# Kernel tuning notes

Hardware: AMD Instinct MI355X
Metric: run time of the kernel (lower is better)

The kernel has to match this reference:

```python
import jax, jax.numpy as jnp
import numpy as np

D_MODEL = 1024
N_HEADS = 16
HEAD_DIM = D_MODEL // N_HEADS


def setup_inputs() -> dict:
    key = jax.random.key(0)
    ks = jax.random.split(key, 9)
    B, S = 4, 2048
    x = jax.random.normal(ks[0], (B, S, D_MODEL), dtype=jnp.float32)
    init = 1.0 / np.sqrt(D_MODEL)
    def lin(kw, kb):
        W = jax.random.uniform(kw, (D_MODEL, D_MODEL), jnp.float32, -init, init)
        b = jax.random.uniform(kb, (D_MODEL,), jnp.float32, -init, init)
        return W, b
    Wq, bq = lin(ks[1], ks[2])
    Wk, bk = lin(ks[3], ks[4])
    Wv, bv = lin(ks[5], ks[6])
    Wo, bo = lin(ks[7], ks[8])
    return {"x": x, "Wq": Wq, "bq": bq, "Wk": Wk, "bk": bk,
            "Wv": Wv, "bv": bv, "Wo": Wo, "bo": bo}


def reference(x, Wq, bq, Wk, bk, Wv, bv, Wo, bo):
    B, S, _ = x.shape
    scale = jnp.sqrt(jnp.float32(HEAD_DIM))
    def split_heads(t):  # [B,S,D] -> [B,H,S,hd]
        return t.reshape(B, S, N_HEADS, HEAD_DIM).transpose(0, 2, 1, 3)
    q = split_heads(x @ Wq.T + bq)
    k = split_heads(x @ Wk.T + bk)
    v = split_heads(x @ Wv.T + bv)
    attn = jnp.einsum('bhqd,bhkd->bhqk', q, k) / scale
    attn = jax.nn.softmax(attn, axis=-1)
    out = jnp.einsum('bhqk,bhkd->bhqd', attn, v)  # [B,H,S,hd]
    out = out.transpose(0, 2, 1, 3).reshape(B, S, D_MODEL)
    return out @ Wo.T + bo
```

## Files before the change

### kernel.cpp

```cpp
#include <hip/hip_runtime.h>
#include <hip/hip_bf16.h>
#include <stdint.h>

typedef __attribute__((ext_vector_type(8))) short bf16x8;
typedef __attribute__((ext_vector_type(4))) float f32x4;
typedef __attribute__((ext_vector_type(16))) float f32x16;
typedef __attribute__((ext_vector_type(2))) unsigned int u32x2;
typedef unsigned short u16;

#define DEVI static __device__ __forceinline__

DEVI u16 f2bf(float f) {
  union { float f; uint32_t u; } x; x.f = f;
  uint32_t r = (x.u + 0x7FFFu + ((x.u >> 16) & 1u)) >> 16;
  return (u16)r;
}

DEVI void gload_lds16(const void* g, void* lds) {
  __builtin_amdgcn_global_load_lds(
      (const __attribute__((address_space(1))) void*)(void*)g,
      (__attribute__((address_space(3))) void*)lds, 16, 0, 0);
}

DEVI unsigned ldsaddr(const void* p) { return (unsigned)(uintptr_t)p; }

__global__ void cvt_all_kernel(const float* __restrict__ x,
                               const float* __restrict__ Wq, const float* __restrict__ Wk,
                               const float* __restrict__ Wv, const float* __restrict__ Wo,
                               const float* __restrict__ bq, const float* __restrict__ bk,
                               const float* __restrict__ bv,
                               u16* __restrict__ xb, u16* __restrict__ Wqkvb,
                               u16* __restrict__ Wob, float* __restrict__ bqkv) {
  const int X4 = 2097152;
  const int W4 = 262144;
  const int total = X4 + 4 * W4 + 768;
  int i = blockIdx.x * blockDim.x + threadIdx.x;
  const int stride = gridDim.x * blockDim.x;
  for (; i < total; i += stride) {
    if (i < X4) {
      float4 v = ((const float4*)x)[i];
      ((ushort4*)xb)[i] = make_ushort4(f2bf(v.x), f2bf(v.y), f2bf(v.z), f2bf(v.w));
    } else if (i < X4 + 4 * W4) {
      int j = i - X4;
      int which = j >> 18;
      int o = j & (W4 - 1);
      const float* src = which == 0 ? Wq : which == 1 ? Wk : which == 2 ? Wv : Wo;
      u16* dst = (which == 3) ? Wob : (Wqkvb + (size_t)which * 1048576);
      float4 v = ((const float4*)src)[o];
      ((ushort4*)dst)[o] = make_ushort4(f2bf(v.x), f2bf(v.y), f2bf(v.z), f2bf(v.w));
    } else {
      int j = i - X4 - 4 * W4;
      int which = j >> 8;
      int o = j & 255;
      const float* src = which == 0 ? bq : which == 1 ? bk : bv;
      ((float4*)bqkv)[which * 256 + o] = ((const float4*)src)[o];
    }
  }
}

template<int OUT_BF16>
__global__ __launch_bounds__(256, 2)
void gemm_bt_kernel(const u16* __restrict__ A, const u16* __restrict__ B,
                    const float* __restrict__ bias, void* __restrict__ C,
                    int M, int N, int K, int scale_cols, float scale_val) {
  __shared__ u16 As[128 * 32];
  __shared__ u16 Bs[128 * 32];
  const int tid = threadIdx.x;
  const int l = tid & 63;
  const int w = tid >> 6;
  const int bm = blockIdx.y, bn = blockIdx.x;
  const int wm = w >> 1, wn = w & 1;

  f32x4 acc[4][4] = {};

  const int srow = w * 32 + (l >> 2);
  const int scol = (l & 3) * 8;
  const u16* gA0 = A + (size_t)(bm * 128 + srow) * K + scol;
  const u16* gA1 = gA0 + (size_t)16 * K;
  const u16* gB0 = B + (size_t)(bn * 128 + srow) * K + scol;
  const u16* gB1 = gB0 + (size_t)16 * K;
  u16* lA0 = As + w * 1024;
  u16* lA1 = As + w * 1024 + 512;
  u16* lB0 = Bs + w * 1024;
  u16* lB1 = Bs + w * 1024 + 512;

  const int ar = wm * 64 + (l & 15);
  const int br = wn * 64 + (l & 15);
  const int kb = (l >> 4) * 8;

  for (int k0 = 0; k0 < K; k0 += 32) {
    __syncthreads();
    gload_lds16(gA0 + k0, lA0);
    gload_lds16(gA1 + k0, lA1);
    gload_lds16(gB0 + k0, lB0);
    gload_lds16(gB1 + k0, lB1);
    __syncthreads();
    bf16x8 af[4], bfr[4];
#pragma unroll
    for (int mf = 0; mf < 4; ++mf)
      af[mf] = *(const bf16x8*)&As[(ar + mf * 16) * 32 + kb];
#pragma unroll
    for (int nf = 0; nf < 4; ++nf)
      bfr[nf] = *(const bf16x8*)&Bs[(br + nf * 16) * 32 + kb];
#pragma unroll
    for (int mf = 0; mf < 4; ++mf)
#pragma unroll
      for (int nf = 0; nf < 4; ++nf)
        acc[mf][nf] = __builtin_amdgcn_mfma_f32_16x16x32_bf16(af[mf], bfr[nf], acc[mf][nf], 0, 0, 0);
  }

  const int rbase = bm * 128 + wm * 64 + (l >> 4) * 4;
  const int cbase = bn * 128 + wn * 64 + (l & 15);
#pragma unroll
  for (int nf = 0; nf < 4; ++nf) {
    int col = cbase + nf * 16;
    float bsv = bias[col];
    float sc = (col < scale_cols) ? scale_val : 1.0f;
#pragma unroll
    for (int mf = 0; mf < 4; ++mf) {
#pragma unroll
      for (int j = 0; j < 4; ++j) {
        int row = rbase + mf * 16 + j;
        float v = (acc[mf][nf][j] + bsv) * sc;
        if (OUT_BF16) ((u16*)C)[(size_t)row * N + col] = f2bf(v);
        else          ((float*)C)[(size_t)row * N + col] = v;
      }
    }
  }
}

DEVI void softmax_pa(f32x16& sA, f32x16& sB, bf16x8* pa, float& lsum, int hi) {
  float rs = 0.f;
#pragma unroll
  for (int r = 0; r < 16; ++r) { sA[r] = __builtin_amdgcn_exp2f(sA[r]); rs += sA[r]; }
#pragma unroll
  for (int r = 0; r < 16; ++r) { sB[r] = __builtin_amdgcn_exp2f(sB[r]); rs += sB[r]; }
  lsum += rs + __shfl_xor(rs, 32, 64);
#pragma unroll
  for (int i = 0; i < 4; ++i) {
    float p0 = (8 * i + 0 < 16) ? sA[(8 * i + 0) & 15] : sB[(8 * i + 0) & 15];
    float p1 = (8 * i + 1 < 16) ? sA[(8 * i + 1) & 15] : sB[(8 * i + 1) & 15];
    float p2 = (8 * i + 2 < 16) ? sA[(8 * i + 2) & 15] : sB[(8 * i + 2) & 15];
    float p3 = (8 * i + 3 < 16) ? sA[(8 * i + 3) & 15] : sB[(8 * i + 3) & 15];
    float p4 = (8 * i + 4 < 16) ? sA[(8 * i + 4) & 15] : sB[(8 * i + 4) & 15];
    float p5 = (8 * i + 5 < 16) ? sA[(8 * i + 5) & 15] : sB[(8 * i + 5) & 15];
    float p6 = (8 * i + 6 < 16) ? sA[(8 * i + 6) & 15] : sB[(8 * i + 6) & 15];
    float p7 = (8 * i + 7 < 16) ? sA[(8 * i + 7) & 15] : sB[(8 * i + 7) & 15];
    unsigned a0, a1, b0, b1;
    asm("v_cvt_pk_bf16_f32 %0, %1, %2" : "=v"(a0) : "v"(p0), "v"(p1));
    asm("v_cvt_pk_bf16_f32 %0, %1, %2" : "=v"(a1) : "v"(p2), "v"(p3));
    asm("v_cvt_pk_bf16_f32 %0, %1, %2" : "=v"(b0) : "v"(p4), "v"(p5));
    asm("v_cvt_pk_bf16_f32 %0, %1, %2" : "=v"(b1) : "v"(p6), "v"(p7));
    unsigned t0 = hi ? a0 : b0;
    unsigned t1 = hi ? a1 : b1;
    unsigned x0 = (unsigned)__shfl_xor((int)t0, 32, 64);
    unsigned x1 = (unsigned)__shfl_xor((int)t1, 32, 64);
    union { unsigned u[4]; bf16x8 v; } U;
    U.u[0] = hi ? x0 : a0;
    U.u[1] = hi ? x1 : a1;
    U.u[2] = hi ? b0 : x0;
    U.u[3] = hi ? b1 : x1;
    pa[i] = U.v;
  }
}

__global__ __launch_bounds__(256, 2)
void attn_kernel(const u16* __restrict__ QKV, u16* __restrict__ O) {
  __shared__ u16 Ks[2][4096];
  __shared__ u16 Vs[2][4096];

  const int tid = threadIdx.x;
  const int l = tid & 63, w = tid >> 6;
  const int hi = l >> 5, c = l & 31;
  const int bh = blockIdx.y, b = bh >> 4, h = bh & 15;
  const int qb = blockIdx.x * 256 + w * 64;
  const size_t rowbase = (size_t)b * 2048;

  bf16x8 qf0[4], qf1[4];
  {
    const u16* Qp0 = QKV + (rowbase + qb + c) * 3072 + h * 64 + hi * 8;
    const u16* Qp1 = QKV + (rowbase + qb + 32 + c) * 3072 + h * 64 + hi * 8;
#pragma unroll
    for (int kk = 0; kk < 4; ++kk) {
      qf0[kk] = *(const bf16x8*)(Qp0 + kk * 16);
      qf1[kk] = *(const bf16x8*)(Qp1 + kk * 16);
    }
  }

  const int kd0 = (w * 2 + 0) * 64 + l;
  const int kd1 = (w * 2 + 1) * 64 + l;
  const int rK0 = kd0 >> 3, dbK0 = (kd0 & 7) ^ (rK0 & 7);
  const int rK1 = kd1 >> 3, dbK1 = (kd1 & 7) ^ (rK1 & 7);
  const u16* srcK0 = QKV + (rowbase + rK0) * 3072 + 1024 + h * 64 + dbK0 * 8;
  const u16* srcK1 = QKV + (rowbase + rK1) * 3072 + 1024 + h * 64 + dbK1 * 8;
  const int kV0 = (kd0 >> 5) * 4 + ((kd0 >> 1) & 3), dV0 = ((kd0 >> 3) & 3) * 16 + (kd0 & 1) * 8;
  const int kV1 = (kd1 >> 5) * 4 + ((kd1 >> 1) & 3), dV1 = ((kd1 >> 3) & 3) * 16 + (kd1 & 1) * 8;
  const u16* srcV0 = QKV + (rowbase + kV0) * 3072 + 2048 + h * 64 + dV0;
  const u16* srcV1 = QKV + (rowbase + kV1) * 3072 + 2048 + h * 64 + dV1;

#define STAGE(buf, tile) { \
    const size_t koff = (size_t)(tile) * 64 * 3072; \
    gload_lds16(srcK0 + koff, &Ks[buf][(w * 2 + 0) * 512]); \
    gload_lds16(srcK1 + koff, &Ks[buf][(w * 2 + 1) * 512]); \
    gload_lds16(srcV0 + koff, &Vs[buf][(w * 2 + 0) * 512]); \
    gload_lds16(srcV1 + koff, &Vs[buf][(w * 2 + 1) * 512]); \
  }

  int koffs[4];
#pragma unroll
  for (int kk = 0; kk < 4; ++kk) koffs[kk] = (((kk * 2 + hi) ^ (c & 7)) * 8);
  const int kbase = c * 64;

  const unsigned vbase = ldsaddr(&Vs[0][0]) + (unsigned)(hi * 1024 + (c >> 4) * 128 + (c & 15) * 8);

  f32x16 o00 = {0,0,0,0,0,0,0,0,0,0,0,0,0,0,0,0};
  f32x16 o01 = {0,0,0,0,0,0,0,0,0,0,0,0,0,0,0,0};
  f32x16 o10 = {0,0,0,0,0,0,0,0,0,0,0,0,0,0,0,0};
  f32x16 o11 = {0,0,0,0,0,0,0,0,0,0,0,0,0,0,0,0};
  float lsum0 = 0.f, lsum1 = 0.f;

  STAGE(0, 0);
  __syncthreads();

  for (int t = 0; t < 32; ++t) {
    const int cur = t & 1;
    if (t < 31) STAGE(cur ^ 1, t + 1);

    const u16* kp = &Ks[cur][0];
    bf16x8 kf[2][4];
#pragma unroll
    for (int kb = 0; kb < 2; ++kb)
#pragma unroll
      for (int kk = 0; kk < 4; ++kk)
        kf[kb][kk] = *(const bf16x8*)&kp[kbase + kb * 2048 + koffs[kk]];

    f32x16 sA0 = {0,0,0,0,0,0,0,0,0,0,0,0,0,0,0,0};
    f32x16 sB0 = {0,0,0,0,0,0,0,0,0,0,0,0,0,0,0,0};
    f32x16 sA1 = {0,0,0,0,0,0,0,0,0,0,0,0,0,0,0,0};
    f32x16 sB1 = {0,0,0,0,0,0,0,0,0,0,0,0,0,0,0,0};
#pragma unroll
    for (int kk = 0; kk < 4; ++kk) {
      sA0 = __builtin_amdgcn_mfma_f32_32x32x16_bf16(kf[0][kk], qf0[kk], sA0, 0, 0, 0);
      sB0 = __builtin_amdgcn_mfma_f32_32x32x16_bf16(kf[1][kk], qf0[kk], sB0, 0, 0, 0);
      sA1 = __builtin_amdgcn_mfma_f32_32x32x16_bf16(kf[0][kk], qf1[kk], sA1, 0, 0, 0);
      sB1 = __builtin_amdgcn_mfma_f32_32x32x16_bf16(kf[1][kk], qf1[kk], sB1, 0, 0, 0);
    }

    const unsigned va = vbase + (unsigned)(cur * 8192);
    u32x2 tt[4][4];
#pragma unroll
    for (int ks = 0; ks < 4; ++ks) {
      unsigned va_ks = va + (unsigned)(ks * 2048);
      asm volatile("ds_read_b64_tr_b16 %0, %1 offset:0"   : "=v"(tt[ks][0]) : "v"(va_ks));
      asm volatile("ds_read_b64_tr_b16 %0, %1 offset:512" : "=v"(tt[ks][1]) : "v"(va_ks));
      asm volatile("ds_read_b64_tr_b16 %0, %1 offset:256" : "=v"(tt[ks][2]) : "v"(va_ks));
      asm volatile("ds_read_b64_tr_b16 %0, %1 offset:768" : "=v"(tt[ks][3]) : "v"(va_ks));
    }

    bf16x8 pa0[4];
    softmax_pa(sA0, sB0, pa0, lsum0, hi);

    asm volatile("s_waitcnt lgkmcnt(0)" ::: "memory");
    __builtin_amdgcn_sched_barrier(0);

#pragma unroll
    for (int ks = 0; ks < 4; ++ks) {
      union { u32x2 d2[2]; bf16x8 v; } V0, V1;
      V0.d2[0] = tt[ks][0]; V0.d2[1] = tt[ks][1];
      V1.d2[0] = tt[ks][2]; V1.d2[1] = tt[ks][3];
      o00 = __builtin_amdgcn_mfma_f32_32x32x16_bf16(pa0[ks], V0.v, o00, 0, 0, 0);
      o01 = __builtin_amdgcn_mfma_f32_32x32x16_bf16(pa0[ks], V1.v, o01, 0, 0, 0);
    }

    bf16x8 pa1[4];
    softmax_pa(sA1, sB1, pa1, lsum1, hi);

#pragma unroll
    for (int ks = 0; ks < 4; ++ks) {
      union { u32x2 d2[2]; bf16x8 v; } V0, V1;
      V0.d2[0] = tt[ks][0]; V0.d2[1] = tt[ks][1];
      V1.d2[0] = tt[ks][2]; V1.d2[1] = tt[ks][3];
      o10 = __builtin_amdgcn_mfma_f32_32x32x16_bf16(pa1[ks], V0.v, o10, 0, 0, 0);
      o11 = __builtin_amdgcn_mfma_f32_32x32x16_bf16(pa1[ks], V1.v, o11, 0, 0, 0);
    }

    __syncthreads();
  }

  u16* Op0 = O + (rowbase + qb) * 1024 + h * 64 + c;
  u16* Op1 = O + (rowbase + qb + 32) * 1024 + h * 64 + c;
#pragma unroll
  for (int r = 0; r < 16; ++r) {
    int q = (r & 3) + 8 * (r >> 2) + 4 * hi;
    float inv0 = 1.0f / __shfl(lsum0, q, 64);
    float inv1 = 1.0f / __shfl(lsum1, q, 64);
    Op0[(size_t)q * 1024]      = f2bf(o00[r] * inv0);
    Op0[(size_t)q * 1024 + 32] = f2bf(o01[r] * inv0);
    Op1[(size_t)q * 1024]      = f2bf(o10[r] * inv1);
    Op1[(size_t)q * 1024 + 32] = f2bf(o11[r] * inv1);
  }
#undef STAGE
}

extern "C" void kernel_launch(void* const* d_in, const int* in_sizes, int n_in,
                              void* d_out, int out_size, void* d_ws, size_t ws_size,
                              hipStream_t stream) {
  const float* x  = (const float*)d_in[0];
  const float* Wq = (const float*)d_in[1];
  const float* bq = (const float*)d_in[2];
  const float* Wk = (const float*)d_in[3];
  const float* bk = (const float*)d_in[4];
  const float* Wv = (const float*)d_in[5];
  const float* bv = (const float*)d_in[6];
  const float* Wo = (const float*)d_in[7];
  const float* bo = (const float*)d_in[8];
  float* out = (float*)d_out;

  char* ws = (char*)d_ws;
  u16*   xb    = (u16*)(ws);
  u16*   Wqkvb = (u16*)(ws + 16777216);
  u16*   Wob   = (u16*)(ws + 23068672);
  float* bqkv  = (float*)(ws + 25165824);
  u16*   QKV   = (u16*)(ws + 25178112);
  u16*   Oa    = (u16*)(ws + 75509760);

  cvt_all_kernel<<<2048, 256, 0, stream>>>(x, Wq, Wk, Wv, Wo, bq, bk, bv,
                                           xb, Wqkvb, Wob, bqkv);

  gemm_bt_kernel<1><<<dim3(24, 64), 256, 0, stream>>>(xb, Wqkvb, bqkv, QKV,
                                                      8192, 3072, 1024, 1024,
                                                      0.125f * 1.4426950408889634f);
  attn_kernel<<<dim3(8, 64), 256, 0, stream>>>(QKV, Oa);
  gemm_bt_kernel<0><<<dim3(8, 64), 256, 0, stream>>>(Oa, Wob, bo, out,
                                                     8192, 1024, 1024, 0, 1.0f);
}
```

Before: 195.7 us.

## Split attention over two key halves and merge partial outputs in a separate kernel

The attention kernel gains a third grid dimension that splits the key/value sequence into two halves. Each block handles 16 key tiles and writes an unnormalized bf16 partial output plus per-row softmax sums to scratch buffers that reuse dead workspace. A new merge kernel adds the two partials and divides by the combined sum. The aim is more parallel blocks and shorter per-block loops, at the cost of an extra launch, extra global traffic, and an extra bf16 rounding of the partials.

```diff
diff --git a/kernel.cpp b/kernel.cpp
--- a/kernel.cpp
+++ b/kernel.cpp
@@ -14,6 +14,10 @@
   union { float f; uint32_t u; } x; x.f = f;
   uint32_t r = (x.u + 0x7FFFu + ((x.u >> 16) & 1u)) >> 16;
   return (u16)r;
+}
+
+DEVI float bf2f(u16 v) {
+  union { uint32_t u; float f; } x; x.u = ((uint32_t)v) << 16; return x.f;
 }
 
 DEVI void gload_lds16(const void* g, void* lds) {
@@ -165,7 +169,8 @@
 }
 
 __global__ __launch_bounds__(256, 2)
-void attn_kernel(const u16* __restrict__ QKV, u16* __restrict__ O) {
+void attn_kernel(const u16* __restrict__ QKV, u16* __restrict__ P0, u16* __restrict__ P1,
+                 float* __restrict__ Ls) {
   __shared__ u16 Ks[2][4096];
   __shared__ u16 Vs[2][4096];
 
@@ -173,8 +178,10 @@
   const int l = tid & 63, w = tid >> 6;
   const int hi = l >> 5, c = l & 31;
   const int bh = blockIdx.y, b = bh >> 4, h = bh & 15;
+  const int kh = blockIdx.z;
   const int qb = blockIdx.x * 256 + w * 64;
   const size_t rowbase = (size_t)b * 2048;
+  const int krow0 = kh << 10;
 
   bf16x8 qf0[4], qf1[4];
   {
@@ -191,12 +198,12 @@
   const int kd1 = (w * 2 + 1) * 64 + l;
   const int rK0 = kd0 >> 3, dbK0 = (kd0 & 7) ^ (rK0 & 7);
   const int rK1 = kd1 >> 3, dbK1 = (kd1 & 7) ^ (rK1 & 7);
-  const u16* srcK0 = QKV + (rowbase + rK0) * 3072 + 1024 + h * 64 + dbK0 * 8;
-  const u16* srcK1 = QKV + (rowbase + rK1) * 3072 + 1024 + h * 64 + dbK1 * 8;
+  const u16* srcK0 = QKV + (rowbase + krow0 + rK0) * 3072 + 1024 + h * 64 + dbK0 * 8;
+  const u16* srcK1 = QKV + (rowbase + krow0 + rK1) * 3072 + 1024 + h * 64 + dbK1 * 8;
   const int kV0 = (kd0 >> 5) * 4 + ((kd0 >> 1) & 3), dV0 = ((kd0 >> 3) & 3) * 16 + (kd0 & 1) * 8;
   const int kV1 = (kd1 >> 5) * 4 + ((kd1 >> 1) & 3), dV1 = ((kd1 >> 3) & 3) * 16 + (kd1 & 1) * 8;
-  const u16* srcV0 = QKV + (rowbase + kV0) * 3072 + 2048 + h * 64 + dV0;
-  const u16* srcV1 = QKV + (rowbase + kV1) * 3072 + 2048 + h * 64 + dV1;
+  const u16* srcV0 = QKV + (rowbase + krow0 + kV0) * 3072 + 2048 + h * 64 + dV0;
+  const u16* srcV1 = QKV + (rowbase + krow0 + kV1) * 3072 + 2048 + h * 64 + dV1;
 
 #define STAGE(buf, tile) { \
     const size_t koff = (size_t)(tile) * 64 * 3072; \
@@ -222,9 +229,9 @@
   STAGE(0, 0);
   __syncthreads();
 
-  for (int t = 0; t < 32; ++t) {
+  for (int t = 0; t < 16; ++t) {
     const int cur = t & 1;
-    if (t < 31) STAGE(cur ^ 1, t + 1);
+    if (t < 15) STAGE(cur ^ 1, t + 1);
 
     const u16* kp = &Ks[cur][0];
     bf16x8 kf[2][4];
@@ -287,19 +294,48 @@
     __syncthreads();
   }
 
-  u16* Op0 = O + (rowbase + qb) * 1024 + h * 64 + c;
-  u16* Op1 = O + (rowbase + qb + 32) * 1024 + h * 64 + c;
+  u16* Pp = kh ? P1 : P0;
+  u16* Op0 = Pp + (rowbase + qb) * 1024 + h * 64 + c;
+  u16* Op1 = Pp + (rowbase + qb + 32) * 1024 + h * 64 + c;
 #pragma unroll
   for (int r = 0; r < 16; ++r) {
     int q = (r & 3) + 8 * (r >> 2) + 4 * hi;
-    float inv0 = 1.0f / __shfl(lsum0, q, 64);
-    float inv1 = 1.0f / __shfl(lsum1, q, 64);
-    Op0[(size_t)q * 1024]      = f2bf(o00[r] * inv0);
-    Op0[(size_t)q * 1024 + 32] = f2bf(o01[r] * inv0);
-    Op1[(size_t)q * 1024]      = f2bf(o10[r] * inv1);
-    Op1[(size_t)q * 1024 + 32] = f2bf(o11[r] * inv1);
+    Op0[(size_t)q * 1024]      = f2bf(o00[r]);
+    Op0[(size_t)q * 1024 + 32] = f2bf(o01[r]);
+    Op1[(size_t)q * 1024]      = f2bf(o10[r]);
+    Op1[(size_t)q * 1024 + 32] = f2bf(o11[r]);
+  }
+  if (!hi) {
+    float* Lp = Ls + (size_t)(kh * 64 + bh) * 2048;
+    Lp[qb + c]      = lsum0;
+    Lp[qb + 32 + c] = lsum1;
   }
 #undef STAGE
+}
+
+__global__ void attn_merge_kernel(const u16* __restrict__ P0, u16* __restrict__ P1,
+                                  const float* __restrict__ Ls) {
+  int i = blockIdx.x * blockDim.x + threadIdx.x;
+  int row = i >> 7;
+  int chunk = i & 127;
+  int h = chunk >> 3;
+  int s = row & 2047;
+  int bh = (row >> 11) * 16 + h;
+  float l0 = Ls[(size_t)bh * 2048 + s];
+  float l1 = Ls[(size_t)(64 + bh) * 2048 + s];
+  float inv = 1.0f / (l0 + l1);
+  const ushort4* a4 = (const ushort4*)(P0 + (size_t)i * 8);
+  ushort4* b4 = (ushort4*)(P1 + (size_t)i * 8);
+  ushort4 a0 = a4[0], a1 = a4[1];
+  ushort4 b0 = b4[0], b1 = b4[1];
+  b4[0] = make_ushort4(f2bf((bf2f(a0.x) + bf2f(b0.x)) * inv),
+                       f2bf((bf2f(a0.y) + bf2f(b0.y)) * inv),
+                       f2bf((bf2f(a0.z) + bf2f(b0.z)) * inv),
+                       f2bf((bf2f(a0.w) + bf2f(b0.w)) * inv));
+  b4[1] = make_ushort4(f2bf((bf2f(a1.x) + bf2f(b1.x)) * inv),
+                       f2bf((bf2f(a1.y) + bf2f(b1.y)) * inv),
+                       f2bf((bf2f(a1.z) + bf2f(b1.z)) * inv),
+                       f2bf((bf2f(a1.w) + bf2f(b1.w)) * inv));
 }
 
 extern "C" void kernel_launch(void* const* d_in, const int* in_sizes, int n_in,
@@ -324,13 +360,18 @@
   u16*   QKV   = (u16*)(ws + 25178112);
   u16*   Oa    = (u16*)(ws + 75509760);
 
+  u16*   P0 = xb;
+  float* Ls = (float*)(ws + 16777216);
+  u16*   P1 = Oa;
+
   cvt_all_kernel<<<2048, 256, 0, stream>>>(x, Wq, Wk, Wv, Wo, bq, bk, bv,
                                            xb, Wqkvb, Wob, bqkv);
 
   gemm_bt_kernel<1><<<dim3(24, 64), 256, 0, stream>>>(xb, Wqkvb, bqkv, QKV,
                                                       8192, 3072, 1024, 1024,
                                                       0.125f * 1.4426950408889634f);
-  attn_kernel<<<dim3(8, 64), 256, 0, stream>>>(QKV, Oa);
+  attn_kernel<<<dim3(8, 64, 2), 256, 0, stream>>>(QKV, P0, P1, Ls);
+  attn_merge_kernel<<<4096, 256, 0, stream>>>(P0, P1, Ls);
   gemm_bt_kernel<0><<<dim3(8, 64), 256, 0, stream>>>(Oa, Wob, bo, out,
                                                      8192, 1024, 1024, 0, 1.0f);
 }
```

Result: slower. 209.9 us (+7.3%).
